# Kernel tuning notes

Hardware: AMD Instinct MI355X
Metric: run time of the kernel (lower is better)

## Reference

```python
import jax, jax.numpy as jnp
import numpy as np

K = 64
N = 1000000
J = 100000
B = 1048576


def setup_inputs() -> dict:
    key = jax.random.key(0)
    k1, k2, k3, k4, k5, k6, k7 = jax.random.split(key, 7)
    users = jax.random.randint(k1, (B,), 0, N, dtype=jnp.int64) if jax.config.jax_enable_x64 else jax.random.randint(k1, (B,), 0, N, dtype=jnp.int32)
    jokes = jax.random.randint(k2, (B,), 0, J, dtype=jnp.int64) if jax.config.jax_enable_x64 else jax.random.randint(k2, (B,), 0, J, dtype=jnp.int32)
    U = jax.random.normal(k3, (N, K), dtype=jnp.float32)
    V = jax.random.normal(k4, (J, K), dtype=jnp.float32)
    a = jax.random.normal(k5, (N, 1), dtype=jnp.float32)
    b = jax.random.normal(k6, (J, 1), dtype=jnp.float32)
    g = jax.random.normal(k7, (1,), dtype=jnp.float32)
    return {"users": users, "jokes": jokes, "U": U, "V": V, "a": a, "b": b, "g": g}


def reference(users, jokes, U, V, a, b, g):
    # gather latent factors and biases, fused dot + bias adds
    u = U[users]              # [B, K]
    v = V[jokes]              # [B, K]
    dot = jnp.sum(u * v, axis=-1)          # per-row dot product (bmm equivalent)
    r = dot + a[users, 0] + b[jokes, 0] + g  # broadcasts g:[1] -> [B]
    return r
```

## Files before the change

### kernel.cpp

```cpp
#include <hip/hip_runtime.h>


constexpr int KDIM = 64;
constexpr int KV   = KDIM / 4;
constexpr int RPG  = 4;

__global__ __launch_bounds__(256) void latent_linear_kernel(
    const int* __restrict__ users,
    const int* __restrict__ jokes,
    const float* __restrict__ U,
    const float* __restrict__ V,
    const float* __restrict__ a,
    const float* __restrict__ b,
    const float* __restrict__ g,
    float* __restrict__ out,
    int B)
{
    const int tid  = blockIdx.x * blockDim.x + threadIdx.x;
    const int grp  = tid >> 4;
    const int sub  = tid & 15;
    const int base = grp * RPG;
    if (base >= B) return;

    const float4* __restrict__ U4 = reinterpret_cast<const float4*>(U);
    const float4* __restrict__ V4 = reinterpret_cast<const float4*>(V);

    const float g0 = g[0];

    if (base + RPG <= B) {
        const int4 u4 = reinterpret_cast<const int4*>(users)[grp];
        const int4 j4 = reinterpret_cast<const int4*>(jokes)[grp];
        const int ui[RPG] = {u4.x, u4.y, u4.z, u4.w};
        const int ji[RPG] = {j4.x, j4.y, j4.z, j4.w};

        float4 uu[RPG], vv[RPG];
#pragma unroll
        for (int r = 0; r < RPG; ++r) uu[r] = U4[(size_t)ui[r] * KV + sub];
#pragma unroll
        for (int r = 0; r < RPG; ++r) vv[r] = V4[(size_t)ji[r] * KV + sub];

#pragma unroll
        for (int r = 0; r < RPG; ++r) {
            float d = uu[r].x * vv[r].x + uu[r].y * vv[r].y
                    + uu[r].z * vv[r].z + uu[r].w * vv[r].w;
            d += __shfl_down(d, 8, 16);
            d += __shfl_down(d, 4, 16);
            d += __shfl_down(d, 2, 16);
            d += __shfl_down(d, 1, 16);
            if (sub == 0)
                out[base + r] = d + a[ui[r]] + b[ji[r]] + g0;
        }
    } else {
        for (int r = 0; r < RPG && base + r < B; ++r) {
            const int row = base + r;
            const int ui = users[row], ji = jokes[row];
            const float4 uu = U4[(size_t)ui * KV + sub];
            const float4 vv = V4[(size_t)ji * KV + sub];
            float d = uu.x * vv.x + uu.y * vv.y + uu.z * vv.z + uu.w * vv.w;
            d += __shfl_down(d, 8, 16);
            d += __shfl_down(d, 4, 16);
            d += __shfl_down(d, 2, 16);
            d += __shfl_down(d, 1, 16);
            if (sub == 0)
                out[row] = d + a[ui] + b[ji] + g0;
        }
    }
}

extern "C" void kernel_launch(void* const* d_in, const int* in_sizes, int n_in,
                              void* d_out, int out_size, void* d_ws, size_t ws_size,
                              hipStream_t stream)
{
    const int*   users = (const int*)d_in[0];
    const int*   jokes = (const int*)d_in[1];
    const float* U     = (const float*)d_in[2];
    const float* V     = (const float*)d_in[3];
    const float* a     = (const float*)d_in[4];
    const float* b     = (const float*)d_in[5];
    const float* g     = (const float*)d_in[6];
    float*       out   = (float*)d_out;

    const int B = in_sizes[0];
    const int groups = (B + RPG - 1) / RPG;
    const long long threads_total = (long long)groups * 16;
    const int block = 256;
    const int grid = (int)((threads_total + block - 1) / block);

    latent_linear_kernel<<<grid, block, 0, stream>>>(users, jokes, U, V, a, b, g, out, B);
}
```

Measured before the change: 382.8 us.

## Use grid-stride persistent loop with prefetched indices and hoisted bias loads

Switches to a fixed grid of 2048 blocks that loop over row groups in grid-stride order. The next group's user and joke indices are prefetched while the current gathers are in flight, and the a/b bias loads are issued before the shuffle reduction. The tail rows are handled serially by a single thread. This aims to cut block launch overhead and hide index-load latency, but it lowers the number of resident waves available to hide gather latency.

```diff
diff --git a/kernel.cpp b/kernel.cpp
--- a/kernel.cpp
+++ b/kernel.cpp
@@ -1,9 +1,8 @@
 #include <hip/hip_runtime.h>
 
 
-constexpr int KDIM = 64;
-constexpr int KV   = KDIM / 4;
-constexpr int RPG  = 4;
+constexpr int KV  = 16;
+constexpr int RPG = 4;
 
 __global__ __launch_bounds__(256) void latent_linear_kernel(
     const int* __restrict__ users,
@@ -16,29 +15,60 @@
     float* __restrict__ out,
     int B)
 {
-    const int tid  = blockIdx.x * blockDim.x + threadIdx.x;
-    const int grp  = tid >> 4;
-    const int sub  = tid & 15;
-    const int base = grp * RPG;
-    if (base >= B) return;
+    const int sub        = threadIdx.x & 15;
+    const int grp_local  = threadIdx.x >> 4;
+    const int grps_per_b = blockDim.x >> 4;
+    const int grp_stride = gridDim.x * grps_per_b;
+    const int ngroups    = B / RPG;
 
     const float4* __restrict__ U4 = reinterpret_cast<const float4*>(U);
     const float4* __restrict__ V4 = reinterpret_cast<const float4*>(V);
+    const int4*   __restrict__ users4 = reinterpret_cast<const int4*>(users);
+    const int4*   __restrict__ jokes4 = reinterpret_cast<const int4*>(jokes);
 
     const float g0 = g[0];
 
-    if (base + RPG <= B) {
-        const int4 u4 = reinterpret_cast<const int4*>(users)[grp];
-        const int4 j4 = reinterpret_cast<const int4*>(jokes)[grp];
+    int grp = blockIdx.x * grps_per_b + grp_local;
+
+    if (blockIdx.x == 0 && threadIdx.x == 0) {
+        for (int row = ngroups * RPG; row < B; ++row) {
+            const int ui = users[row], ji = jokes[row];
+            float d = 0.f;
+            for (int k = 0; k < 64; ++k) d += U[(size_t)ui * 64 + k] * V[(size_t)ji * 64 + k];
+            out[row] = d + a[ui] + b[ji] + g0;
+        }
+    }
+
+    if (grp >= ngroups) return;
+
+    int4 u4 = users4[grp];
+    int4 j4 = jokes4[grp];
+
+    while (grp < ngroups) {
         const int ui[RPG] = {u4.x, u4.y, u4.z, u4.w};
         const int ji[RPG] = {j4.x, j4.y, j4.z, j4.w};
 
         float4 uu[RPG], vv[RPG];
 #pragma unroll
-        for (int r = 0; r < RPG; ++r) uu[r] = U4[(size_t)ui[r] * KV + sub];
+        for (int r = 0; r < RPG; ++r) {
+            uu[r] = U4[(size_t)ui[r] * KV + sub];
+            vv[r] = V4[(size_t)ji[r] * KV + sub];
+        }
+
+        float ab[RPG], bb[RPG];
 #pragma unroll
-        for (int r = 0; r < RPG; ++r) vv[r] = V4[(size_t)ji[r] * KV + sub];
+        for (int r = 0; r < RPG; ++r) {
+            ab[r] = a[ui[r]];
+            bb[r] = b[ji[r]];
+        }
 
+        const int next = grp + grp_stride;
+        if (next < ngroups) {
+            u4 = users4[next];
+            j4 = jokes4[next];
+        }
+
+        const int base = grp * RPG;
 #pragma unroll
         for (int r = 0; r < RPG; ++r) {
             float d = uu[r].x * vv[r].x + uu[r].y * vv[r].y
@@ -48,22 +78,10 @@
             d += __shfl_down(d, 2, 16);
             d += __shfl_down(d, 1, 16);
             if (sub == 0)
-                out[base + r] = d + a[ui[r]] + b[ji[r]] + g0;
+                out[base + r] = d + ab[r] + bb[r] + g0;
         }
-    } else {
-        for (int r = 0; r < RPG && base + r < B; ++r) {
-            const int row = base + r;
-            const int ui = users[row], ji = jokes[row];
-            const float4 uu = U4[(size_t)ui * KV + sub];
-            const float4 vv = V4[(size_t)ji * KV + sub];
-            float d = uu.x * vv.x + uu.y * vv.y + uu.z * vv.z + uu.w * vv.w;
-            d += __shfl_down(d, 8, 16);
-            d += __shfl_down(d, 4, 16);
-            d += __shfl_down(d, 2, 16);
-            d += __shfl_down(d, 1, 16);
-            if (sub == 0)
-                out[row] = d + a[ui] + b[ji] + g0;
-        }
+
+        grp = next;
     }
 }
 
@@ -81,10 +99,12 @@
     float*       out   = (float*)d_out;
 
     const int B = in_sizes[0];
-    const int groups = (B + RPG - 1) / RPG;
-    const long long threads_total = (long long)groups * 16;
+
     const int block = 256;
-    const int grid = (int)((threads_total + block - 1) / block);
+    int grid = 2048;
+    const int ngroups = B / RPG;
+    const int max_grid = (ngroups + (block / 16) - 1) / (block / 16);
+    if (grid > max_grid) grid = max_grid > 0 ? max_grid : 1;
 
     latent_linear_kernel<<<grid, block, 0, stream>>>(users, jokes, U, V, a, b, g, out, B);
 }
```

After: 387.3 us. Within noise of the previous version (+1.2%).
